# Kernel tuning notes

Measured on AMD Instinct MI355X. Metric: run time of the kernel, lower is better.

## Reference

```python
import jax, jax.numpy as jnp
import numpy as np

EPS = 1e-6

def _layernorm2d(x, w, b):
    # normalize over channel dim (axis=1) per (b,h,w)
    u = jnp.mean(x, axis=1, keepdims=True)
    s = jnp.mean((x - u) ** 2, axis=1, keepdims=True)
    xn = (x - u) / jnp.sqrt(s + EPS)
    return xn * w[None, :, None, None] + b[None, :, None, None]

def _conv1x1(x, w, b):
    # w: (O, C, 1, 1)
    y = jnp.einsum('bchw,oc->bohw', x, w[:, :, 0, 0])
    return y + b[None, :, None, None]

def _dwconv3x3(x, w):
    # w: (C, 1, 3, 3), groups = C, padding 1, no bias
    C = x.shape[1]
    return jax.lax.conv_general_dilated(
        x, w, window_strides=(1, 1), padding=((1, 1), (1, 1)),
        dimension_numbers=('NCHW', 'OIHW', 'NCHW'), feature_group_count=C)

def _linrec_scan(a, u, axis):
    # s_t = a_t * s_{t-1} + u_t via associative scan
    def comb(l, r):
        al, ul = l
        ar, ur = r
        return al * ar, ar * ul + ur
    return jax.lax.associative_scan(comb, (a, u), axis=axis)[1]

def _bidir_scan(z, a, b, g, axis):
    u = b * z
    s_f = _linrec_scan(a, u, axis)
    s_b = jnp.flip(_linrec_scan(jnp.flip(a, axis), jnp.flip(u, axis), axis), axis)
    return g * (s_f + s_b)

def setup_inputs() -> dict:
    key = jax.random.key(0)
    ks = jax.random.split(key, 6)
    B, C, H, W = 8, 192, 128, 128
    x = jax.random.normal(ks[0], (B, C, H, W), dtype=jnp.float32)
    ln_w = jnp.ones((C,), jnp.float32)
    ln_b = jnp.zeros((C,), jnp.float32)
    dw_w = jax.random.normal(ks[1], (C, 1, 3, 3), jnp.float32) * (1.0 / 3.0)
    loc_w = jax.random.normal(ks[2], (C, C, 1, 1), jnp.float32) * (1.0 / np.sqrt(C))
    loc_b = jnp.zeros((C,), jnp.float32)
    par_w = jax.random.normal(ks[3], (3 * C, C, 1, 1), jnp.float32) * (1.0 / np.sqrt(C))
    par_b = jnp.zeros((3 * C,), jnp.float32)
    out_w = jax.random.normal(ks[4], (C, C, 1, 1), jnp.float32) * (1.0 / np.sqrt(C))
    out_b = jnp.zeros((C,), jnp.float32)
    return {"x": x, "ln_w": ln_w, "ln_b": ln_b, "dw_w": dw_w,
            "loc_w": loc_w, "loc_b": loc_b, "par_w": par_w, "par_b": par_b,
            "out_w": out_w, "out_b": out_b}

def reference(x, ln_w, ln_b, dw_w, loc_w, loc_b, par_w, par_b, out_w, out_b):
    C = x.shape[1]
    z = _layernorm2d(x, ln_w, ln_b)
    local_feat = _conv1x1(_dwconv3x3(z, dw_w), loc_w, loc_b)
    gates = _conv1x1(z, par_w, par_b)
    alpha = jax.nn.sigmoid(gates[:, :C])
    beta = jax.nn.sigmoid(gates[:, C:2 * C])
    gamma = jax.nn.sigmoid(gates[:, 2 * C:])
    y_w = _bidir_scan(z, alpha, beta, gamma, axis=3)  # along W
    y_h = _bidir_scan(z, alpha, beta, gamma, axis=2)  # along H
    y = local_feat + 0.5 * (y_w + y_h)
    y = jax.nn.silu(y)
    y = _conv1x1(y, out_w, out_b)
    return x + y
```

## Files before the change

kernel.cpp:

```cpp
#include <hip/hip_runtime.h>
#include <cstdint>
#include <cstddef>

#define B 8
#define C 192
#define H 128
#define W 128
#define HW (H * W)
#define CHW ((size_t)C * HW)
#define K C

typedef __attribute__((ext_vector_type(8))) short short8v;
typedef __attribute__((ext_vector_type(4))) float f32x4;
typedef __attribute__((ext_vector_type(4))) unsigned short ushort4v;

__device__ __forceinline__ float bf2f(unsigned short s) {
    union { float f; unsigned u; } cv; cv.u = ((unsigned)s) << 16; return cv.f;
}
__device__ __forceinline__ unsigned short f2bf(float f) {
    union { float f; unsigned u; } cv; cv.f = f;
    unsigned r = (cv.u + 0x7fffu + ((cv.u >> 16) & 1u)) >> 16;
    return (unsigned short)r;
}

__global__ void prepack_kernel(const float* __restrict__ pw, const float* __restrict__ lw,
                               const float* __restrict__ ow, unsigned short* __restrict__ wb) {
    int i = blockIdx.x * 256 + threadIdx.x;
    const int NPW = 3 * C * K, NL = C * K;
    if (i < NPW) wb[i] = f2bf(pw[i]);
    else if (i < NPW + NL) wb[i] = f2bf(lw[i - NPW]);
    else if (i < NPW + 2 * NL) wb[i] = f2bf(ow[i - NPW - NL]);
}

__global__ void ln_kernel(const float* __restrict__ x, const float* __restrict__ lw,
                          const float* __restrict__ lb, unsigned short* __restrict__ zt,
                          unsigned short* __restrict__ zn) {
    int p = blockIdx.x * 256 + threadIdx.x;
    int b = p >> 14, hw = p & 16383;
    const float* xp = x + (size_t)b * CHW + hw;
    float sum = 0.f, sq = 0.f;
    for (int c = 0; c < C; ++c) {
        float v = xp[(size_t)c * HW];
        sum += v; sq += v * v;
    }
    float mean = sum * (1.0f / C);
    float var = fmaxf(sq * (1.0f / C) - mean * mean, 0.f);
    float rs = rsqrtf(var + 1e-6f);
    unsigned short* zp = zt + (size_t)p * K;
    unsigned short* znp = zn + (size_t)b * CHW + hw;
#pragma unroll 4
    for (int c8 = 0; c8 < K / 8; ++c8) {
        short8v v;
#pragma unroll
        for (int j = 0; j < 8; ++j) {
            int c = c8 * 8 + j;
            float r = (xp[(size_t)c * HW] - mean) * rs * lw[c] + lb[c];
            unsigned short rb = f2bf(r);
            v[j] = (short)rb;
            znp[(size_t)c * HW] = rb;
        }
        *(short8v*)(zp + c8 * 8) = v;
    }
}

template <int MODE>
__global__ __launch_bounds__(256, 4)
void conv_mfma_kernel(const unsigned short* __restrict__ zt, const unsigned short* __restrict__ yin,
                      const unsigned short* __restrict__ zn,
                      const unsigned short* __restrict__ wb, const float* __restrict__ bias,
                      const float* __restrict__ xres, float* __restrict__ Pf,
                      unsigned short* __restrict__ PA, unsigned short* __restrict__ PU,
                      unsigned short* __restrict__ PG) {
    __shared__ char smem[96 * 384];
    int tid = threadIdx.x;
    int lane = tid & 63, wv = tid >> 6;
    int p0 = blockIdx.x * 128 + wv * 32;
    int lr = lane & 15, lh = lane >> 4;
    int sw = (lr & 7) << 4;

    short8v bfr[2][6];
    if (MODE != 2) {
#pragma unroll
        for (int s = 0; s < 2; ++s) {
            const unsigned short* zr = zt + (size_t)(p0 + s * 16 + lr) * K + lh * 8;
#pragma unroll
            for (int t = 0; t < 6; ++t) bfr[s][t] = *(const short8v*)(zr + t * 32);
        }
    } else {
        int bl = p0 >> 14, hwb = p0 & 16383;
        const unsigned short* yb = yin + (size_t)bl * CHW;
#pragma unroll
        for (int s = 0; s < 2; ++s) {
            int hw = hwb + s * 16 + lr;
#pragma unroll
            for (int t = 0; t < 6; ++t) {
                int c0 = t * 32 + lh * 8;
                short8v v;
#pragma unroll
                for (int j = 0; j < 8; ++j)
                    v[j] = (short)yb[(size_t)(c0 + j) * HW + hw];
                bfr[s][t] = v;
            }
        }
    }

    const int NGY = (MODE == 0) ? 3 : 1;
    for (int gy = 0; gy < NGY; ++gy) {
        for (int hf = 0; hf < 2; ++hf) {
            __syncthreads();
            const unsigned short* wsrc = wb + (size_t)gy * C * K + (size_t)hf * 96 * K;
#pragma unroll
            for (int it = 0; it < 9; ++it) {
                int e8 = it * 256 + tid;
                int row = e8 / 24;
                int cb = (e8 % 24) * 16;
                short8v v = *(const short8v*)(wsrc + e8 * 8);
                *(short8v*)(smem + row * 384 + (cb ^ ((row & 7) << 4))) = v;
            }
            __syncthreads();

            for (int otl = 0; otl < 6; ++otl) {
                int ot = hf * 6 + otl;
                int rb = (otl * 16 + lr) * 384;
                int o = ot * 16 + lr;
                f32x4 acc[2];
#pragma unroll
                for (int s = 0; s < 2; ++s) acc[s] = (f32x4){0.f, 0.f, 0.f, 0.f};
#pragma unroll
                for (int t = 0; t < 6; ++t) {
                    short8v af = *(const short8v*)(smem + rb + ((t * 64 + lh * 16) ^ sw));
#pragma unroll
                    for (int s = 0; s < 2; ++s)
                        acc[s] = __builtin_amdgcn_mfma_f32_16x16x32_bf16(bfr[s][t], af, acc[s], 0, 0, 0);
                }
                float bi = bias[(MODE == 0 ? gy * C : 0) + o];
#pragma unroll
                for (int s = 0; s < 2; ++s) {
                    int pst = p0 + s * 16 + lh * 4;
                    int bl = pst >> 14, hw = pst & 16383;
                    if (MODE == 0) {
                        ushort4v q;
                        ushort4v z4;
                        if (gy == 1)
                            z4 = *(const ushort4v*)(zn + (size_t)bl * CHW + (size_t)o * HW + hw);
#pragma unroll
                        for (int j = 0; j < 4; ++j) {
                            float v = acc[s][j] + bi;
                            v = 1.f / (1.f + __expf(-v));
                            if (gy == 1) v *= bf2f(z4[j]);
                            q[j] = f2bf(v);
                        }
                        unsigned short* dst = (gy == 0) ? PA : ((gy == 1) ? PU : PG);
                        *(ushort4v*)(dst + (size_t)bl * CHW + (size_t)o * HW + hw) = q;
                    } else if (MODE == 1) {
                        ushort4v q;
#pragma unroll
                        for (int j = 0; j < 4; ++j) q[j] = f2bf(acc[s][j] + bi);
                        *(ushort4v*)(PA + (size_t)bl * CHW + (size_t)o * HW + hw) = q;
                    } else {
                        size_t ad = (size_t)bl * CHW + (size_t)o * HW + hw;
                        f32x4 x4 = *(const f32x4*)(xres + ad);
                        f32x4 q;
#pragma unroll
                        for (int j = 0; j < 4; ++j) q[j] = acc[s][j] + bi + x4[j];
                        *(f32x4*)(Pf + ad) = q;
                    }
                }
            }
        }
    }
}

#define TROWS 180
#define LPAD  392
__global__ __launch_bounds__(256, 2)
void dw3x3_kernel(const unsigned short* __restrict__ zt, const float* __restrict__ wgt,
                  unsigned short* __restrict__ dt) {
    __shared__ char lds[TROWS * LPAD];
    int tid = threadIdx.x;
    int bx = blockIdx.x;
    int bimg = bx >> 7;
    int rem = bx & 127;
    int th = rem >> 3, tw = rem & 7;
    int h0 = th * 8, w0 = tw * 16;
    size_t ibase = (size_t)bimg * HW;

    for (int e = tid; e < TROWS * 24; e += 256) {
        int row = e / 24, ch = e % 24;
        int hh = row / 18, ww = row % 18;
        int h = h0 - 1 + hh, w = w0 - 1 + ww;
        short8v v;
        if (h >= 0 && h < H && w >= 0 && w < W)
            v = *(const short8v*)(zt + (ibase + h * W + w) * K + ch * 8);
        else
            v = (short8v){0, 0, 0, 0, 0, 0, 0, 0};
        *(short8v*)(lds + row * LPAD + ch * 16) = v;
    }
    __syncthreads();

    int w_l = tid & 15, h_l = (tid >> 4) & 7, half = tid >> 7;
    int p_out = (h0 + h_l) * W + (w0 + w_l);
    unsigned short* dp = dt + (ibase + p_out) * K + half * 96;
#pragma unroll
    for (int cc = 0; cc < 12; ++cc) {
        int c8 = half * 12 + cc;
        float acc[8];
#pragma unroll
        for (int j = 0; j < 8; ++j) acc[j] = 0.f;
#pragma unroll
        for (int dy = -1; dy <= 1; ++dy) {
#pragma unroll
            for (int dx = -1; dx <= 1; ++dx) {
                int row = (h_l + 1 + dy) * 18 + (w_l + 1 + dx);
                short8v zv = *(const short8v*)(lds + row * LPAD + c8 * 16);
                int t = (dy + 1) * 3 + (dx + 1);
#pragma unroll
                for (int j = 0; j < 8; ++j)
                    acc[j] += wgt[(c8 * 8 + j) * 9 + t] * bf2f((unsigned short)zv[j]);
            }
        }
        short8v ov;
#pragma unroll
        for (int j = 0; j < 8; ++j) ov[j] = (short)f2bf(acc[j]);
        *(short8v*)(dp + cc * 8) = ov;
    }
}

__global__ __launch_bounds__(1024)
void scan_fused_kernel(const unsigned short* __restrict__ A_, const unsigned short* __restrict__ U_,
                       const unsigned short* __restrict__ G_, unsigned short* __restrict__ LY) {
    extern __shared__ float SMEM[];
    float* Sl = SMEM;
    unsigned* AU = (unsigned*)(SMEM + HW);
    float* CA = SMEM + 2 * HW;
    float* CU = CA + 1056;
    float* DA = CU + 1056;
    float* DU = DA + 1056;
    int tid = threadIdx.x;
    size_t pb = (size_t)blockIdx.x * HW;

    int h = tid >> 3, wc = tid & 7;
    int swzA = (h & 7) << 2;
    unsigned au[16];
    {
        const unsigned short* ap = A_ + pb + h * W + wc * 16;
        const unsigned short* up = U_ + pb + h * W + wc * 16;
        short8v a0 = *(const short8v*)ap, a1 = *(const short8v*)(ap + 8);
        short8v u0 = *(const short8v*)up, u1 = *(const short8v*)(up + 8);
#pragma unroll
        for (int i = 0; i < 8; ++i) {
            au[i]     = (unsigned)(unsigned short)a0[i] | ((unsigned)(unsigned short)u0[i] << 16);
            au[8 + i] = (unsigned)(unsigned short)a1[i] | ((unsigned)(unsigned short)u1[i] << 16);
        }
    }
#pragma unroll
    for (int i = 0; i < 16; ++i)
        AU[h * 128 + ((wc * 16 + i) ^ swzA)] = au[i];
    {
        float Af = 1.f, Uf = 0.f, Ab = 1.f, Ub = 0.f;
#pragma unroll
        for (int i = 0; i < 16; ++i) {
            float a = bf2f(au[i] & 0xffff), u = bf2f(au[i] >> 16);
            Uf = a * Uf + u; Af *= a;
        }
#pragma unroll
        for (int i = 15; i >= 0; --i) {
            float a = bf2f(au[i] & 0xffff), u = bf2f(au[i] >> 16);
            Ub = a * Ub + u; Ab *= a;
        }
        CA[wc * 132 + h] = Af; CU[wc * 132 + h] = Uf;
        DA[wc * 132 + h] = Ab; DU[wc * 132 + h] = Ub;
    }
    __syncthreads();

    if (tid < 128) {
        float s = 0.f;
#pragma unroll
        for (int k = 0; k < 8; ++k) {
            float Aa = CA[k * 132 + tid], Uu = CU[k * 132 + tid];
            CU[k * 132 + tid] = s;
            s = Aa * s + Uu;
        }
    } else if (tid < 256) {
        int hh = tid - 128;
        float s = 0.f;
#pragma unroll
        for (int k = 7; k >= 0; --k) {
            float Aa = DA[k * 132 + hh], Uu = DU[k * 132 + hh];
            DU[k * 132 + hh] = s;
            s = Aa * s + Uu;
        }
    }
    __syncthreads();

    {
        float sf = CU[wc * 132 + h];
        float sfa[16];
#pragma unroll
        for (int i = 0; i < 16; ++i) {
            float a = bf2f(au[i] & 0xffff), u = bf2f(au[i] >> 16);
            sf = a * sf + u; sfa[i] = sf;
        }
        float sb = DU[wc * 132 + h];
#pragma unroll
        for (int i = 15; i >= 0; --i) {
            float a = bf2f(au[i] & 0xffff), u = bf2f(au[i] >> 16);
            sb = a * sb + u;
            Sl[h * W + ((wc * 16 + i) ^ swzA)] = sfa[i] + sb;
        }
    }
    __syncthreads();

    int w = tid & 127, hc = tid >> 7;
    int h0 = hc * 16;
    unsigned au2[16];
#pragma unroll
    for (int i = 0; i < 16; ++i) {
        int hh = h0 + i;
        au2[i] = AU[hh * 128 + (w ^ ((hh & 7) << 2))];
    }
    {
        float Af = 1.f, Uf = 0.f, Ab = 1.f, Ub = 0.f;
#pragma unroll
        for (int i = 0; i < 16; ++i) {
            float a = bf2f(au2[i] & 0xffff), u = bf2f(au2[i] >> 16);
            Uf = a * Uf + u; Af *= a;
        }
#pragma unroll
        for (int i = 15; i >= 0; --i) {
            float a = bf2f(au2[i] & 0xffff), u = bf2f(au2[i] >> 16);
            Ub = a * Ub + u; Ab *= a;
        }
        CA[hc * 132 + w] = Af; CU[hc * 132 + w] = Uf;
        DA[hc * 132 + w] = Ab; DU[hc * 132 + w] = Ub;
    }
    __syncthreads();

    if (tid < 128) {
        float s = 0.f;
#pragma unroll
        for (int k = 0; k < 8; ++k) {
            float Aa = CA[k * 132 + tid], Uu = CU[k * 132 + tid];
            CU[k * 132 + tid] = s;
            s = Aa * s + Uu;
        }
    } else if (tid < 256) {
        int ww = tid - 128;
        float s = 0.f;
#pragma unroll
        for (int k = 7; k >= 0; --k) {
            float Aa = DA[k * 132 + ww], Uu = DU[k * 132 + ww];
            DU[k * 132 + ww] = s;
            s = Aa * s + Uu;
        }
    }
    __syncthreads();

    {
        float sf = CU[hc * 132 + w];
        float sfa[16];
#pragma unroll
        for (int i = 0; i < 16; ++i) {
            float a = bf2f(au2[i] & 0xffff), u = bf2f(au2[i] >> 16);
            sf = a * sf + u; sfa[i] = sf;
        }
        float sb = DU[hc * 132 + w];
#pragma unroll
        for (int i = 15; i >= 0; --i) {
            float a = bf2f(au2[i] & 0xffff), u = bf2f(au2[i] >> 16);
            sb = a * sb + u;
            int hh = h0 + i;
            size_t off = pb + (size_t)hh * W + w;
            float g = bf2f(G_[off]);
            float wsum = Sl[hh * W + (w ^ ((hh & 7) << 2))];
            float v = bf2f(LY[off]) + 0.5f * g * (wsum + sfa[i] + sb);
            LY[off] = f2bf(v / (1.f + __expf(-v)));
        }
    }
}

extern "C" void kernel_launch(void* const* d_in, const int* in_sizes, int n_in,
                              void* d_out, int out_size, void* d_ws, size_t ws_size,
                              hipStream_t stream) {
    const float* x     = (const float*)d_in[0];
    const float* ln_w  = (const float*)d_in[1];
    const float* ln_b  = (const float*)d_in[2];
    const float* dw_w  = (const float*)d_in[3];
    const float* loc_w = (const float*)d_in[4];
    const float* loc_b = (const float*)d_in[5];
    const float* par_w = (const float*)d_in[6];
    const float* par_b = (const float*)d_in[7];
    const float* out_w = (const float*)d_in[8];
    const float* out_b = (const float*)d_in[9];
    float* out = (float*)d_out;
    unsigned short* wsu = (unsigned short*)d_ws;

    const int WBN = 5 * C * K;
    int nb = 8;
    while (nb > 1) {
        size_t need = (size_t)WBN * 2 + (size_t)5 * nb * CHW * 2;
        if (need <= ws_size) break;
        nb >>= 1;
    }

    prepack_kernel<<<(WBN + 255) / 256, 256, 0, stream>>>(par_w, loc_w, out_w, wsu);

    const size_t SCAN_LDS = (size_t)(2 * HW + 4 * 1056) * 4;

    for (int b0 = 0; b0 < B; b0 += nb) {
        size_t ge = (size_t)nb * CHW;
        unsigned short* WB = wsu;
        unsigned short* Ab = wsu + WBN;
        unsigned short* Ub = Ab + ge;
        unsigned short* Gb = Ub + ge;
        unsigned short* ZT = Gb + ge;
        unsigned short* DT = ZT + ge;
        const float* xg = x + (size_t)b0 * CHW;
        int npg = nb * HW;

        ln_kernel<<<npg / 256, 256, 0, stream>>>(xg, ln_w, ln_b, ZT, DT);
        conv_mfma_kernel<0><<<npg / 128, 256, 0, stream>>>(
            ZT, nullptr, DT, WB, par_b, nullptr, nullptr, Ab, Ub, Gb);
        dw3x3_kernel<<<nb * 128, 256, 0, stream>>>(ZT, dw_w, DT);
        conv_mfma_kernel<1><<<npg / 128, 256, 0, stream>>>(
            DT, nullptr, nullptr, WB + 3 * C * K, loc_b, nullptr, nullptr, ZT, nullptr, nullptr);
        scan_fused_kernel<<<nb * C, 1024, SCAN_LDS, stream>>>(Ab, Ub, Gb, ZT);
        conv_mfma_kernel<2><<<npg / 128, 256, 0, stream>>>(
            nullptr, ZT, nullptr, WB + 4 * C * K, out_b, xg, out + (size_t)b0 * CHW,
            nullptr, nullptr, nullptr);
    }
}
```

Baseline: 358.0 us.

## Fuse LayerNorm into gate projection MFMA kernel, drop channel-major z copy

Merges the LayerNorm kernel with the gate 1x1-conv MFMA kernel. Each block computes per-pixel statistics across channels with a two-way split reduction, normalizes straight into MFMA operand registers, and writes only the pixel-major ZT copy. The channel-major z buffer write and its re-read in the gating epilogue go away, along with one kernel launch and the ZT re-read. The trade-off is that x is read twice inside the fused kernel, and the u-gate epilogue now does strided scalar gathers from ZT.

After: 327.3 us. 8.6% less time.

```diff
diff --git a/kernel.cpp b/kernel.cpp
--- a/kernel.cpp
+++ b/kernel.cpp
@@ -32,45 +32,125 @@
     else if (i < NPW + 2 * NL) wb[i] = f2bf(ow[i - NPW - NL]);
 }
 
-__global__ void ln_kernel(const float* __restrict__ x, const float* __restrict__ lw,
-                          const float* __restrict__ lb, unsigned short* __restrict__ zt,
-                          unsigned short* __restrict__ zn) {
-    int p = blockIdx.x * 256 + threadIdx.x;
-    int b = p >> 14, hw = p & 16383;
-    const float* xp = x + (size_t)b * CHW + hw;
-    float sum = 0.f, sq = 0.f;
-    for (int c = 0; c < C; ++c) {
-        float v = xp[(size_t)c * HW];
-        sum += v; sq += v * v;
-    }
-    float mean = sum * (1.0f / C);
-    float var = fmaxf(sq * (1.0f / C) - mean * mean, 0.f);
-    float rs = rsqrtf(var + 1e-6f);
-    unsigned short* zp = zt + (size_t)p * K;
-    unsigned short* znp = zn + (size_t)b * CHW + hw;
-#pragma unroll 4
-    for (int c8 = 0; c8 < K / 8; ++c8) {
-        short8v v;
-#pragma unroll
-        for (int j = 0; j < 8; ++j) {
-            int c = c8 * 8 + j;
-            float r = (xp[(size_t)c * HW] - mean) * rs * lw[c] + lb[c];
-            unsigned short rb = f2bf(r);
-            v[j] = (short)rb;
-            znp[(size_t)c * HW] = rb;
-        }
-        *(short8v*)(zp + c8 * 8) = v;
+__global__ __launch_bounds__(256, 4)
+void lngates_kernel(const float* __restrict__ x, const float* __restrict__ lw,
+                    const float* __restrict__ lb, const unsigned short* __restrict__ wb,
+                    const float* __restrict__ bias, unsigned short* __restrict__ ZT,
+                    unsigned short* __restrict__ PA, unsigned short* __restrict__ PU,
+                    unsigned short* __restrict__ PG) {
+    __shared__ char smem[96 * 384];
+    __shared__ float stat[2][128];
+    __shared__ float lwb[2][192];
+    int tid = threadIdx.x;
+    int p0 = blockIdx.x * 128;
+    int bl = p0 >> 14, hwb = p0 & 16383;
+
+    if (tid < 192) { lwb[0][tid] = lw[tid]; lwb[1][tid] = lb[tid]; }
+
+    {
+        float* part = (float*)smem;
+        int px = tid & 127, half = tid >> 7;
+        const float* xp = x + (size_t)bl * CHW + hwb + px;
+        float sum = 0.f, sq = 0.f;
+        for (int c = half * 96; c < half * 96 + 96; ++c) {
+            float v = xp[(size_t)c * HW];
+            sum += v; sq += v * v;
+        }
+        part[half * 128 + px] = sum;
+        part[256 + half * 128 + px] = sq;
+        __syncthreads();
+        if (tid < 128) {
+            float s = part[tid] + part[128 + tid];
+            float q = part[256 + tid] + part[384 + tid];
+            float mean = s * (1.0f / C);
+            float var = fmaxf(q * (1.0f / C) - mean * mean, 0.f);
+            stat[0][tid] = mean;
+            stat[1][tid] = rsqrtf(var + 1e-6f);
+        }
+        __syncthreads();
+    }
+
+    int lane = tid & 63, wv = tid >> 6;
+    int pw0 = p0 + wv * 32;
+    int lr = lane & 15, lh = lane >> 4;
+    int sw = (lr & 7) << 4;
+
+    short8v bfr[2][6];
+#pragma unroll
+    for (int s = 0; s < 2; ++s) {
+        int px = pw0 + s * 16 + lr;
+        int hw = px & 16383;
+        float mean = stat[0][px - p0], rs = stat[1][px - p0];
+        const float* xp = x + (size_t)bl * CHW + hw;
+#pragma unroll
+        for (int t = 0; t < 6; ++t) {
+            short8v v;
+#pragma unroll
+            for (int j = 0; j < 8; ++j) {
+                int c = t * 32 + lh * 8 + j;
+                float r = (xp[(size_t)c * HW] - mean) * rs * lwb[0][c] + lwb[1][c];
+                v[j] = (short)f2bf(r);
+            }
+            bfr[s][t] = v;
+            *(short8v*)(ZT + (size_t)px * K + t * 32 + lh * 8) = v;
+        }
+    }
+
+    for (int gy = 0; gy < 3; ++gy) {
+        for (int hf = 0; hf < 2; ++hf) {
+            __syncthreads();
+            const unsigned short* wsrc = wb + (size_t)gy * C * K + (size_t)hf * 96 * K;
+#pragma unroll
+            for (int it = 0; it < 9; ++it) {
+                int e8 = it * 256 + tid;
+                int row = e8 / 24;
+                int cb = (e8 % 24) * 16;
+                short8v v = *(const short8v*)(wsrc + e8 * 8);
+                *(short8v*)(smem + row * 384 + (cb ^ ((row & 7) << 4))) = v;
+            }
+            __syncthreads();
+
+            for (int otl = 0; otl < 6; ++otl) {
+                int ot = hf * 6 + otl;
+                int rb = (otl * 16 + lr) * 384;
+                int o = ot * 16 + lr;
+                f32x4 acc[2];
+#pragma unroll
+                for (int s = 0; s < 2; ++s) acc[s] = (f32x4){0.f, 0.f, 0.f, 0.f};
+#pragma unroll
+                for (int t = 0; t < 6; ++t) {
+                    short8v af = *(const short8v*)(smem + rb + ((t * 64 + lh * 16) ^ sw));
+#pragma unroll
+                    for (int s = 0; s < 2; ++s)
+                        acc[s] = __builtin_amdgcn_mfma_f32_16x16x32_bf16(bfr[s][t], af, acc[s], 0, 0, 0);
+                }
+                float bi = bias[gy * C + o];
+#pragma unroll
+                for (int s = 0; s < 2; ++s) {
+                    int pst = pw0 + s * 16 + lh * 4;
+                    int hw = pst & 16383;
+                    ushort4v q;
+#pragma unroll
+                    for (int j = 0; j < 4; ++j) {
+                        float v = acc[s][j] + bi;
+                        v = 1.f / (1.f + __expf(-v));
+                        if (gy == 1) v *= bf2f(ZT[(size_t)(pst + j) * K + o]);
+                        q[j] = f2bf(v);
+                    }
+                    unsigned short* dst = (gy == 0) ? PA : ((gy == 1) ? PU : PG);
+                    *(ushort4v*)(dst + (size_t)bl * CHW + (size_t)o * HW + hw) = q;
+                }
+            }
+        }
     }
 }
 
 template <int MODE>
 __global__ __launch_bounds__(256, 4)
 void conv_mfma_kernel(const unsigned short* __restrict__ zt, const unsigned short* __restrict__ yin,
-                      const unsigned short* __restrict__ zn,
                       const unsigned short* __restrict__ wb, const float* __restrict__ bias,
                       const float* __restrict__ xres, float* __restrict__ Pf,
-                      unsigned short* __restrict__ PA, unsigned short* __restrict__ PU,
-                      unsigned short* __restrict__ PG) {
+                      unsigned short* __restrict__ PA) {
     __shared__ char smem[96 * 384];
     int tid = threadIdx.x;
     int lane = tid & 63, wv = tid >> 6;
@@ -104,67 +184,50 @@
         }
     }
 
-    const int NGY = (MODE == 0) ? 3 : 1;
-    for (int gy = 0; gy < NGY; ++gy) {
-        for (int hf = 0; hf < 2; ++hf) {
-            __syncthreads();
-            const unsigned short* wsrc = wb + (size_t)gy * C * K + (size_t)hf * 96 * K;
-#pragma unroll
-            for (int it = 0; it < 9; ++it) {
-                int e8 = it * 256 + tid;
-                int row = e8 / 24;
-                int cb = (e8 % 24) * 16;
-                short8v v = *(const short8v*)(wsrc + e8 * 8);
-                *(short8v*)(smem + row * 384 + (cb ^ ((row & 7) << 4))) = v;
-            }
-            __syncthreads();
-
-            for (int otl = 0; otl < 6; ++otl) {
-                int ot = hf * 6 + otl;
-                int rb = (otl * 16 + lr) * 384;
-                int o = ot * 16 + lr;
-                f32x4 acc[2];
-#pragma unroll
-                for (int s = 0; s < 2; ++s) acc[s] = (f32x4){0.f, 0.f, 0.f, 0.f};
-#pragma unroll
-                for (int t = 0; t < 6; ++t) {
-                    short8v af = *(const short8v*)(smem + rb + ((t * 64 + lh * 16) ^ sw));
-#pragma unroll
-                    for (int s = 0; s < 2; ++s)
-                        acc[s] = __builtin_amdgcn_mfma_f32_16x16x32_bf16(bfr[s][t], af, acc[s], 0, 0, 0);
-                }
-                float bi = bias[(MODE == 0 ? gy * C : 0) + o];
-#pragma unroll
-                for (int s = 0; s < 2; ++s) {
-                    int pst = p0 + s * 16 + lh * 4;
-                    int bl = pst >> 14, hw = pst & 16383;
-                    if (MODE == 0) {
-                        ushort4v q;
-                        ushort4v z4;
-                        if (gy == 1)
-                            z4 = *(const ushort4v*)(zn + (size_t)bl * CHW + (size_t)o * HW + hw);
-#pragma unroll
-                        for (int j = 0; j < 4; ++j) {
-                            float v = acc[s][j] + bi;
-                            v = 1.f / (1.f + __expf(-v));
-                            if (gy == 1) v *= bf2f(z4[j]);
-                            q[j] = f2bf(v);
-                        }
-                        unsigned short* dst = (gy == 0) ? PA : ((gy == 1) ? PU : PG);
-                        *(ushort4v*)(dst + (size_t)bl * CHW + (size_t)o * HW + hw) = q;
-                    } else if (MODE == 1) {
-                        ushort4v q;
-#pragma unroll
-                        for (int j = 0; j < 4; ++j) q[j] = f2bf(acc[s][j] + bi);
-                        *(ushort4v*)(PA + (size_t)bl * CHW + (size_t)o * HW + hw) = q;
-                    } else {
-                        size_t ad = (size_t)bl * CHW + (size_t)o * HW + hw;
-                        f32x4 x4 = *(const f32x4*)(xres + ad);
-                        f32x4 q;
-#pragma unroll
-                        for (int j = 0; j < 4; ++j) q[j] = acc[s][j] + bi + x4[j];
-                        *(f32x4*)(Pf + ad) = q;
-                    }
+    for (int hf = 0; hf < 2; ++hf) {
+        __syncthreads();
+        const unsigned short* wsrc = wb + (size_t)hf * 96 * K;
+#pragma unroll
+        for (int it = 0; it < 9; ++it) {
+            int e8 = it * 256 + tid;
+            int row = e8 / 24;
+            int cb = (e8 % 24) * 16;
+            short8v v = *(const short8v*)(wsrc + e8 * 8);
+            *(short8v*)(smem + row * 384 + (cb ^ ((row & 7) << 4))) = v;
+        }
+        __syncthreads();
+
+        for (int otl = 0; otl < 6; ++otl) {
+            int ot = hf * 6 + otl;
+            int rb = (otl * 16 + lr) * 384;
+            int o = ot * 16 + lr;
+            f32x4 acc[2];
+#pragma unroll
+            for (int s = 0; s < 2; ++s) acc[s] = (f32x4){0.f, 0.f, 0.f, 0.f};
+#pragma unroll
+            for (int t = 0; t < 6; ++t) {
+                short8v af = *(const short8v*)(smem + rb + ((t * 64 + lh * 16) ^ sw));
+#pragma unroll
+                for (int s = 0; s < 2; ++s)
+                    acc[s] = __builtin_amdgcn_mfma_f32_16x16x32_bf16(bfr[s][t], af, acc[s], 0, 0, 0);
+            }
+            float bi = bias[o];
+#pragma unroll
+            for (int s = 0; s < 2; ++s) {
+                int pst = p0 + s * 16 + lh * 4;
+                int bl = pst >> 14, hw = pst & 16383;
+                if (MODE == 1) {
+                    ushort4v q;
+#pragma unroll
+                    for (int j = 0; j < 4; ++j) q[j] = f2bf(acc[s][j] + bi);
+                    *(ushort4v*)(PA + (size_t)bl * CHW + (size_t)o * HW + hw) = q;
+                } else {
+                    size_t ad = (size_t)bl * CHW + (size_t)o * HW + hw;
+                    f32x4 x4 = *(const f32x4*)(xres + ad);
+                    f32x4 q;
+#pragma unroll
+                    for (int j = 0; j < 4; ++j) q[j] = acc[s][j] + bi + x4[j];
+                    *(f32x4*)(Pf + ad) = q;
                 }
             }
         }
@@ -418,15 +481,13 @@
         const float* xg = x + (size_t)b0 * CHW;
         int npg = nb * HW;
 
-        ln_kernel<<<npg / 256, 256, 0, stream>>>(xg, ln_w, ln_b, ZT, DT);
-        conv_mfma_kernel<0><<<npg / 128, 256, 0, stream>>>(
-            ZT, nullptr, DT, WB, par_b, nullptr, nullptr, Ab, Ub, Gb);
+        lngates_kernel<<<npg / 128, 256, 0, stream>>>(
+            xg, ln_w, ln_b, WB, par_b, ZT, Ab, Ub, Gb);
         dw3x3_kernel<<<nb * 128, 256, 0, stream>>>(ZT, dw_w, DT);
         conv_mfma_kernel<1><<<npg / 128, 256, 0, stream>>>(
-            DT, nullptr, nullptr, WB + 3 * C * K, loc_b, nullptr, nullptr, ZT, nullptr, nullptr);
+            DT, nullptr, WB + 3 * C * K, loc_b, nullptr, nullptr, ZT);
         scan_fused_kernel<<<nb * C, 1024, SCAN_LDS, stream>>>(Ab, Ub, Gb, ZT);
         conv_mfma_kernel<2><<<npg / 128, 256, 0, stream>>>(
-            nullptr, ZT, nullptr, WB + 4 * C * K, out_b, xg, out + (size_t)b0 * CHW,
-            nullptr, nullptr, nullptr);
-    }
-}
+            nullptr, ZT, WB + 4 * C * K, out_b, xg, out + (size_t)b0 * CHW, nullptr);
+    }
+}
```
